# Optimization experiments

Measured on AMD Instinct MI355X. Metric: run time of the kernel, lower is better.

Reference implementation:

```python
import jax, jax.numpy as jnp
import numpy as np

N_NODES = 50000
N_PAIRS_MAP = 4096
N_EDGES = 500000
N_SCORE_PAIRS = 1000000
FEAT = 300   # feature_dim == in_channels
HID = 128    # hidden_channels
HEADS = 3
OUT = 10     # out_channels
NEG_SLOPE = 0.2


def setup_inputs() -> dict:
    key = jax.random.key(0)
    ks = jax.random.split(key, 24)
    s = 0.05
    d = {
        "feature_sub": jax.random.normal(ks[0], (N_PAIRS_MAP, FEAT), jnp.float32),
        "feature_com": jax.random.normal(ks[1], (N_PAIRS_MAP, FEAT), jnp.float32),
        "x": jax.random.normal(ks[2], (N_NODES, FEAT), jnp.float32),
        "com_idx": jax.random.randint(ks[3], (N_PAIRS_MAP,), 0, N_NODES, jnp.int32),
        "edge_index": jax.random.randint(ks[4], (2, N_EDGES), 0, N_NODES, jnp.int32),
        "pair_idx": jax.random.randint(ks[5], (N_SCORE_PAIRS, 2), 0, N_NODES, jnp.int32),
        # cross-attention params
        "Wq": jax.random.normal(ks[6], (FEAT, FEAT), jnp.float32) * s,
        "bq": jnp.zeros((FEAT,), jnp.float32),
        "Wk": jax.random.normal(ks[7], (FEAT, FEAT), jnp.float32) * s,
        "bk": jnp.zeros((FEAT,), jnp.float32),
        "Wv": jax.random.normal(ks[8], (FEAT, FEAT), jnp.float32) * s,
        "bv": jnp.zeros((FEAT,), jnp.float32),
        "Wf": jax.random.normal(ks[9], (FEAT, FEAT), jnp.float32) * s,
        "bf": jnp.zeros((FEAT,), jnp.float32),
        # GATConv layer 1 (heads=3, concat)
        "W1": jax.random.normal(ks[10], (FEAT, HEADS * HID), jnp.float32) * s,
        "a_src1": jax.random.normal(ks[11], (HEADS, HID), jnp.float32) * s,
        "a_dst1": jax.random.normal(ks[12], (HEADS, HID), jnp.float32) * s,
        "b1": jnp.zeros((HEADS * HID,), jnp.float32),
        # GATConv layer 2 (heads=1)
        "W2": jax.random.normal(ks[13], (HEADS * HID, OUT), jnp.float32) * s,
        "a_src2": jax.random.normal(ks[14], (1, OUT), jnp.float32) * s,
        "a_dst2": jax.random.normal(ks[15], (1, OUT), jnp.float32) * s,
        "b2": jnp.zeros((OUT,), jnp.float32),
    }
    return d


def gat_conv(h_in, src, dst, W, a_src, a_dst, b, n_nodes):
    """PyG-style GATConv: self-loops, per-dst softmax attention, sum-aggregate."""
    H, C = a_src.shape
    h = (h_in @ W).reshape(n_nodes, H, C)                     # [N,H,C]
    e_src = jnp.einsum("nhc,hc->nh", h, a_src)                # [N,H]
    e_dst = jnp.einsum("nhc,hc->nh", h, a_dst)                # [N,H]
    # add self-loops
    loops = jnp.arange(n_nodes, dtype=src.dtype)
    src = jnp.concatenate([src, loops])
    dst = jnp.concatenate([dst, loops])
    e = jax.nn.leaky_relu(e_src[src] + e_dst[dst], NEG_SLOPE)  # [E,H]
    m = jax.ops.segment_max(e, dst, num_segments=n_nodes)      # [N,H]
    m = jnp.where(jnp.isfinite(m), m, 0.0)
    ex = jnp.exp(e - m[dst])                                   # [E,H]
    denom = jax.ops.segment_sum(ex, dst, num_segments=n_nodes)  # [N,H]
    alpha = ex / (denom[dst] + 1e-16)                          # [E,H]
    msg = h[src] * alpha[..., None]                            # [E,H,C]
    out = jax.ops.segment_sum(msg, dst, num_segments=n_nodes)  # [N,H,C]
    return out.reshape(n_nodes, H * C) + b


def reference(feature_sub, feature_com, x, com_idx, edge_index, pair_idx,
              Wq, bq, Wk, bk, Wv, bv, Wf, bf,
              W1, a_src1, a_dst1, b1, W2, a_src2, a_dst2, b2):
    # --- compute_attention: cross-attention between sub and com features ---
    q = feature_sub @ Wq + bq                                  # [B,D]
    k = feature_com @ Wk + bk
    v = feature_com @ Wv + bv
    scores = jax.nn.softmax((q @ k.T) / jnp.sqrt(jnp.float32(FEAT)), axis=-1)
    fused = (feature_sub + scores @ v) @ Wf + bf               # [B,D]
    # --- change_node_feature: write fused features into graph node features ---
    x = x.at[com_idx].set(fused)
    # --- linkTrain: GAT1 -> ELU -> GAT2 ---
    src, dst = edge_index[0], edge_index[1]
    h = gat_conv(x, src, dst, W1, a_src1, a_dst1, b1, N_NODES)
    h = jax.nn.elu(h)
    emb = gat_conv(h, src, dst, W2, a_src2, a_dst2, b2, N_NODES)  # [N,OUT]
    # --- per-pair link scores (vectorized gather + batched dot) ---
    scores_out = jnp.sum(emb[pair_idx[:, 0]] * emb[pair_idx[:, 1]], axis=-1)
    return scores_out
```

## Files before the change

kernel.cpp:

```cpp
#include <hip/hip_runtime.h>
#include <math.h>

#define NN      50000
#define BP      4096
#define NE      500000
#define NP      1000000
#define FEAT    300
#define KP      320
#define HID     128
#define HEADS   3
#define OUTC    10
#define HC1     (HEADS*HID)
#define EMBS    12
#define TOTE    (NE+NN)
#define NEG_SLOPE 0.2f

static inline int cdiv(int a, int b) { return (a + b - 1) / b; }

using bfrag = __attribute__((ext_vector_type(8))) short;
using ffrag = __attribute__((ext_vector_type(4))) float;

__device__ inline float leaky(float x) { return x > 0.f ? x : NEG_SLOPE * x; }
__device__ inline unsigned short bf16_rne(float f) {
    unsigned u = __float_as_uint(f);
    unsigned r = u + 0x7FFFu + ((u >> 16) & 1u);
    return (unsigned short)(r >> 16);
}
__device__ inline float bf16f(unsigned short h) { return __uint_as_float(((unsigned)h) << 16); }

__device__ __forceinline__ void gload_lds16(const unsigned short* g, unsigned short* l) {
    __builtin_amdgcn_global_load_lds((const __attribute__((address_space(1))) void*)g,
                                     (__attribute__((address_space(3))) void*)l, 16, 0, 0);
}

__global__ void fill_f32(float* p, float v, long n) {
    long i = (long)blockIdx.x * blockDim.x + threadIdx.x;
    if (i < n) p[i] = v;
}

__global__ void conv_pad8(const float* __restrict__ in, unsigned short* __restrict__ H,
                          unsigned short* __restrict__ L, long M, int K, int Kp) {
    long idx = (long)blockIdx.x * blockDim.x + threadIdx.x;
    int cpk = Kp >> 3;
    long total = M * cpk;
    if (idx >= total) return;
    int chunk = (int)(idx % cpk);
    long row = idx / cpk;
    int k0 = chunk * 8;
    const float* ip = in + row * K;
    float v[8];
    if (k0 + 8 <= K) {
        float4 a = *(const float4*)(ip + k0);
        float4 b = *(const float4*)(ip + k0 + 4);
        v[0]=a.x; v[1]=a.y; v[2]=a.z; v[3]=a.w; v[4]=b.x; v[5]=b.y; v[6]=b.z; v[7]=b.w;
    } else {
#pragma unroll
        for (int j = 0; j < 8; j++) { int k = k0 + j; v[j] = (k < K) ? ip[k] : 0.f; }
    }
    unsigned short hs[8], ls[8];
#pragma unroll
    for (int j = 0; j < 8; j++) {
        unsigned short h = bf16_rne(v[j]);
        hs[j] = h; ls[j] = bf16_rne(v[j] - bf16f(h));
    }
    long o = row * Kp + k0;
    *(uint4*)&H[o] = *(const uint4*)hs;
    *(uint4*)&L[o] = *(const uint4*)ls;
}

__global__ void convT_pad(const float* __restrict__ in, unsigned short* __restrict__ H,
                          unsigned short* __restrict__ L, int K, int N, int Kp) {
    long idx = (long)blockIdx.x * blockDim.x + threadIdx.x;
    long total = (long)N * Kp;
    if (idx >= total) return;
    int k = (int)(idx % Kp);
    long n = idx / Kp;
    float f = (k < K) ? in[(long)k * N + n] : 0.f;
    unsigned short h = bf16_rne(f);
    H[idx] = h;
    L[idx] = bf16_rne(f - bf16f(h));
}

template <int MODE>
__global__ __launch_bounds__(256) void gemm_bf(
    const unsigned short* __restrict__ Ah, const unsigned short* __restrict__ Al, int lda,
    const unsigned short* __restrict__ Bh, const unsigned short* __restrict__ Bl, int ldb,
    const float* __restrict__ bias, const float* __restrict__ addsrc,
    float* __restrict__ C0, unsigned short* __restrict__ H0, unsigned short* __restrict__ L0,
    int M, int N, int K, float scale, int ldo)
{
    __shared__ __align__(16) unsigned short Ahs[4][64][8], Als[4][64][8];
    __shared__ __align__(16) unsigned short Bhs[4][64][8], Bls[4][64][8];
    int t = threadIdx.x, w = t >> 6, l = t & 63, lrow = l & 15, lq = l >> 4;
    int rowBase = blockIdx.y * 64, colBase = blockIdx.x * 64;
    int Kr = (K + 31) & ~31;

    int arow = min(rowBase + l, M - 1);
    int brow = min(colBase + l, N - 1);
    const unsigned short* ga_h = Ah + (long)arow * lda + w * 8;
    const unsigned short* ga_l = Al + (long)arow * lda + w * 8;
    const unsigned short* gb_h = Bh + (long)brow * ldb + w * 8;
    const unsigned short* gb_l = Bl + (long)brow * ldb + w * 8;

    ffrag acc[4] = {{0.f,0.f,0.f,0.f},{0.f,0.f,0.f,0.f},{0.f,0.f,0.f,0.f},{0.f,0.f,0.f,0.f}};

    for (int k0 = 0; k0 < Kr; k0 += 32) {
        *(uint4*)&Ahs[w][l][0] = *(const uint4*)(ga_h + k0);
        *(uint4*)&Als[w][l][0] = *(const uint4*)(ga_l + k0);
        *(uint4*)&Bhs[w][l][0] = *(const uint4*)(gb_h + k0);
        *(uint4*)&Bls[w][l][0] = *(const uint4*)(gb_l + k0);
        __syncthreads();
        bfrag ah  = *(const bfrag*)&Ahs[lq][w * 16 + lrow][0];
        bfrag alo = *(const bfrag*)&Als[lq][w * 16 + lrow][0];
#pragma unroll
        for (int ct = 0; ct < 4; ct++) {
            bfrag bh = *(const bfrag*)&Bhs[lq][ct * 16 + lrow][0];
            bfrag bl = *(const bfrag*)&Bls[lq][ct * 16 + lrow][0];
            acc[ct] = __builtin_amdgcn_mfma_f32_16x16x32_bf16(ah,  bh, acc[ct], 0, 0, 0);
            acc[ct] = __builtin_amdgcn_mfma_f32_16x16x32_bf16(ah,  bl, acc[ct], 0, 0, 0);
            acc[ct] = __builtin_amdgcn_mfma_f32_16x16x32_bf16(alo, bh, acc[ct], 0, 0, 0);
        }
        __syncthreads();
    }

#pragma unroll
    for (int ct = 0; ct < 4; ct++) {
        int gc = colBase + ct * 16 + lrow;
        if (gc >= N) continue;
#pragma unroll
        for (int r = 0; r < 4; r++) {
            int gr = rowBase + w * 16 + lq * 4 + r;
            if (gr >= M) continue;
            float v = acc[ct][r];
            if (MODE == 0) {
                float o = v * scale;
                if (bias) o += bias[gc];
                if (addsrc) o += addsrc[(long)gr * ldo + gc];
                C0[(long)gr * ldo + gc] = o;
            } else if (MODE == 1) {
                float o = v + bias[gc];
                unsigned short h = bf16_rne(o);
                H0[(long)gr * ldo + gc] = h;
                L0[(long)gr * ldo + gc] = bf16_rne(o - bf16f(h));
            } else {
                float o = v + bias[gc];
                unsigned short h = bf16_rne(o);
                H0[(long)gc * ldo + gr] = h;
                L0[(long)gc * ldo + gr] = bf16_rne(o - bf16f(h));
            }
        }
    }
}

template <bool SPLITK, int OUT>
__global__ __launch_bounds__(256) void gemm_gl128(
    const unsigned short* __restrict__ Ah, long dAl, int lda,
    const unsigned short* __restrict__ Bh, long dBl, int ldb,
    float* __restrict__ C0, unsigned short* __restrict__ Hb,
    int M, int N, int K, float scale, int KC)
{
    __shared__ __align__(16) unsigned short As[128][64];
    __shared__ __align__(16) unsigned short Bs[128][64];
    int t = threadIdx.x, w = t >> 6, l = t & 63, lrow = l & 15, lq = l >> 4;
    int wr = w >> 1, wc = w & 1;
    int rowBase = blockIdx.y * 128, colBase = blockIdx.x * 128;
    int Kr = (K + 31) & ~31;
    int kbeg = SPLITK ? blockIdx.z * KC : 0;
    int kend = SPLITK ? min(Kr, kbeg + KC) : Kr;

    bool isA = (w < 2);
    const unsigned short* Mb = isA ? Ah : Bh;
    long dHL = isA ? dAl : dBl;
    int ld   = isA ? lda : ldb;
    int mx   = (isA ? M : N) - 1;
    int rb0  = (isA ? rowBase : colBase) + (w & 1) * 64;
    int lr8  = l >> 3;
    int lg   = (l & 7) ^ lr8;
    long lane_off = (long)((lg & 3) * 8) + ((lg >> 2) ? dHL : 0);
    const unsigned short* gp[8];
#pragma unroll
    for (int i = 0; i < 8; i++) {
        int r = rb0 + i * 8 + lr8;
        gp[i] = Mb + (long)min(r, mx) * ld + lane_off;
    }
    unsigned short* ldst[8];
    {
        unsigned short (*T)[64] = isA ? As : Bs;
#pragma unroll
        for (int i = 0; i < 8; i++) ldst[i] = &T[(w & 1) * 64 + i * 8][0];
    }

    ffrag acc[4][4];
#pragma unroll
    for (int m = 0; m < 4; m++)
#pragma unroll
        for (int n = 0; n < 4; n++) acc[m][n] = ffrag{0.f, 0.f, 0.f, 0.f};

    int arow0 = wr * 64 + lrow, brow0 = wc * 64 + lrow;
    int xr = lrow & 7;
    int sh = ((lq    ) ^ xr) * 8;
    int sl = ((lq + 4) ^ xr) * 8;

    for (int k0 = kbeg; k0 < kend; k0 += 32) {
#pragma unroll
        for (int i = 0; i < 8; i++) gload_lds16(gp[i] + k0, ldst[i]);
        __syncthreads();

        bfrag bh[4], bl[4];
#pragma unroll
        for (int n = 0; n < 4; n++) {
            bh[n] = *(const bfrag*)&Bs[brow0 + n * 16][sh];
            bl[n] = *(const bfrag*)&Bs[brow0 + n * 16][sl];
        }
#pragma unroll
        for (int m = 0; m < 4; m++) {
            bfrag ah = *(const bfrag*)&As[arow0 + m * 16][sh];
            bfrag al = *(const bfrag*)&As[arow0 + m * 16][sl];
#pragma unroll
            for (int n = 0; n < 4; n++) {
                acc[m][n] = __builtin_amdgcn_mfma_f32_16x16x32_bf16(ah, bh[n], acc[m][n], 0, 0, 0);
                acc[m][n] = __builtin_amdgcn_mfma_f32_16x16x32_bf16(ah, bl[n], acc[m][n], 0, 0, 0);
                acc[m][n] = __builtin_amdgcn_mfma_f32_16x16x32_bf16(al, bh[n], acc[m][n], 0, 0, 0);
            }
        }
        __syncthreads();
    }

#pragma unroll
    for (int n = 0; n < 4; n++) {
        int gc = colBase + wc * 64 + n * 16 + lrow;
        if (gc >= N) continue;
#pragma unroll
        for (int m = 0; m < 4; m++) {
#pragma unroll
            for (int r = 0; r < 4; r++) {
                int gr = rowBase + wr * 64 + m * 16 + lq * 4 + r;
                if (gr >= M) continue;
                if (OUT == 0) {
                    float* Cz = SPLITK ? (C0 + (long)blockIdx.z * M * N) : C0;
                    Cz[(long)gr * N + gc] = acc[m][n][r] * scale;
                } else {
                    Hb[(long)gr * N + gc] = bf16_rne(acc[m][n][r]);
                }
            }
        }
    }
}

__global__ __launch_bounds__(256) void softmax_hl(const float* __restrict__ S,
                                                  unsigned short* __restrict__ SH,
                                                  unsigned short* __restrict__ SL) {
    int row = blockIdx.x, tid = threadIdx.x;
    const float* p = S + (long)row * BP + tid * 16;
    float ev[16];
    __shared__ float red[256];
    float m = -1e30f;
#pragma unroll
    for (int i = 0; i < 4; i++) {
        float4 a = *(const float4*)(p + i * 4);
        ev[4*i] = a.x; ev[4*i+1] = a.y; ev[4*i+2] = a.z; ev[4*i+3] = a.w;
        m = fmaxf(m, fmaxf(fmaxf(a.x, a.y), fmaxf(a.z, a.w)));
    }
    red[tid] = m; __syncthreads();
    for (int s = 128; s > 0; s >>= 1) { if (tid < s) red[tid] = fmaxf(red[tid], red[tid + s]); __syncthreads(); }
    m = red[0]; __syncthreads();
    float sum = 0.f;
#pragma unroll
    for (int i = 0; i < 16; i++) { float e = expf(ev[i] - m); ev[i] = e; sum += e; }
    red[tid] = sum; __syncthreads();
    for (int s = 128; s > 0; s >>= 1) { if (tid < s) red[tid] += red[tid + s]; __syncthreads(); }
    float inv = 1.0f / red[0];
    unsigned short hs[16], ls[16];
#pragma unroll
    for (int i = 0; i < 16; i++) {
        float e = ev[i] * inv;
        unsigned short h = bf16_rne(e);
        hs[i] = h; ls[i] = bf16_rne(e - bf16f(h));
    }
    long o = (long)row * BP + tid * 16;
    *(uint4*)&SH[o]     = *(const uint4*)&hs[0];
    *(uint4*)&SH[o + 8] = *(const uint4*)&hs[8];
    *(uint4*)&SL[o]     = *(const uint4*)&ls[0];
    *(uint4*)&SL[o + 8] = *(const uint4*)&ls[8];
}

__global__ void splitk_reduce8(const float* __restrict__ part, const float* __restrict__ resid,
                               unsigned short* __restrict__ H, unsigned short* __restrict__ L,
                               int Mr, int Nc, int Kp2, int sk) {
    long idx = (long)blockIdx.x * blockDim.x + threadIdx.x;
    int cpk = Kp2 >> 3;
    long total = (long)Mr * cpk;
    if (idx >= total) return;
    int chunk = (int)(idx % cpk);
    long row = idx / cpk;
    int c0 = chunk * 8;
    float v[8] = {0.f,0.f,0.f,0.f,0.f,0.f,0.f,0.f};
    if (c0 + 8 <= Nc) {
        long base = row * Nc + c0;
#pragma unroll
        for (int z = 0; z < 8; z++) {
            if (z >= sk) break;
            float4 a = *(const float4*)(part + (long)z * Mr * Nc + base);
            float4 b = *(const float4*)(part + (long)z * Mr * Nc + base + 4);
            v[0]+=a.x; v[1]+=a.y; v[2]+=a.z; v[3]+=a.w; v[4]+=b.x; v[5]+=b.y; v[6]+=b.z; v[7]+=b.w;
        }
        float4 a = *(const float4*)(resid + base);
        float4 b = *(const float4*)(resid + base + 4);
        v[0]+=a.x; v[1]+=a.y; v[2]+=a.z; v[3]+=a.w; v[4]+=b.x; v[5]+=b.y; v[6]+=b.z; v[7]+=b.w;
    } else if (c0 < Nc) {
#pragma unroll
        for (int j = 0; j < 8; j++) {
            int c = c0 + j;
            if (c < Nc) {
                long base = row * Nc + c;
                float s = resid[base];
                for (int z = 0; z < sk; z++) s += part[(long)z * Mr * Nc + base];
                v[j] = s;
            }
        }
    }
    unsigned short hs[8], ls[8];
#pragma unroll
    for (int j = 0; j < 8; j++) {
        unsigned short h = bf16_rne(v[j]);
        hs[j] = h; ls[j] = bf16_rne(v[j] - bf16f(h));
    }
    long o = row * Kp2 + c0;
    *(uint4*)&H[o] = *(const uint4*)hs;
    *(uint4*)&L[o] = *(const uint4*)ls;
}

__global__ void scatter_init(int* last, const int* __restrict__ com, int B) {
    int i = blockIdx.x * blockDim.x + threadIdx.x;
    if (i < B) last[com[i]] = -1;
}
__global__ void scatter_max(int* last, const int* __restrict__ com, int B) {
    int i = blockIdx.x * blockDim.x + threadIdx.x;
    if (i < B) atomicMax(&last[com[i]], i);
}
__global__ void scatter_write_hl(const int* __restrict__ last, const int* __restrict__ com,
                                 const float* __restrict__ fused,
                                 unsigned short* __restrict__ xH, unsigned short* __restrict__ xL, int B) {
    int i = blockIdx.x;
    int node = com[i];
    if (last[node] != i) return;
    for (int c = threadIdx.x; c < KP; c += blockDim.x) {
        float f = (c < FEAT) ? fused[(long)i * FEAT + c] : 0.f;
        unsigned short h = bf16_rne(f);
        xH[(long)node * KP + c] = h;
        xL[(long)node * KP + c] = bf16_rne(f - bf16f(h));
    }
}

__global__ __launch_bounds__(256) void node_attn_coef3(
    const unsigned short* __restrict__ h1, const float* __restrict__ a_src,
    const float* __restrict__ a_dst, float* __restrict__ es, float* __restrict__ ed, int N)
{
    int w = threadIdx.x >> 6, lane = threadIdx.x & 63;
    int n = blockIdx.x * 4 + w;
    if (n >= N) return;
    const unsigned short* hp = h1 + (long)n * HC1;
    float s0 = 0.f, s1 = 0.f, s2 = 0.f, d0 = 0.f, d1 = 0.f, d2 = 0.f;
#pragma unroll
    for (int j = 0; j < 2; j++) {
        int c = lane + 64 * j;
        float v = bf16f(hp[c]);
        s0 = fmaf(v, a_src[c], s0); d0 = fmaf(v, a_dst[c], d0);
        c += 128; v = bf16f(hp[c]);
        s1 = fmaf(v, a_src[c], s1); d1 = fmaf(v, a_dst[c], d1);
        c += 128; v = bf16f(hp[c]);
        s2 = fmaf(v, a_src[c], s2); d2 = fmaf(v, a_dst[c], d2);
    }
#pragma unroll
    for (int off = 32; off > 0; off >>= 1) {
        s0 += __shfl_down(s0, off); s1 += __shfl_down(s1, off); s2 += __shfl_down(s2, off);
        d0 += __shfl_down(d0, off); d1 += __shfl_down(d1, off); d2 += __shfl_down(d2, off);
    }
    if (lane == 0) {
        es[n * 3 + 0] = s0; es[n * 3 + 1] = s1; es[n * 3 + 2] = s2;
        ed[n * 3 + 0] = d0; ed[n * 3 + 1] = d1; ed[n * 3 + 2] = d2;
    }
}

__global__ void deg_init(int* deg, int n) {
    int i = blockIdx.x * blockDim.x + threadIdx.x;
    if (i < n) deg[i] = 1;
}
__global__ void deg_count(const int* __restrict__ dst, int* deg, int E) {
    int e = blockIdx.x * blockDim.x + threadIdx.x;
    if (e < E) atomicAdd(&deg[dst[e]], 1);
}
__global__ void scan_part(const int* __restrict__ deg, int* __restrict__ bsum, int n) {
    __shared__ int red[256];
    int tid = threadIdx.x;
    int i = blockIdx.x * 256 + tid;
    red[tid] = (i < n) ? deg[i] : 0;
    __syncthreads();
    for (int s = 128; s > 0; s >>= 1) { if (tid < s) red[tid] += red[tid + s]; __syncthreads(); }
    if (tid == 0) bsum[blockIdx.x] = red[0];
}
__global__ __launch_bounds__(256) void scan_bsum(int* __restrict__ bsum, int nb) {
    __shared__ int tmp[256];
    int tid = threadIdx.x;
    int v = (tid < nb) ? bsum[tid] : 0;
    tmp[tid] = v; __syncthreads();
    for (int off = 1; off < 256; off <<= 1) {
        int t2 = (tid >= off) ? tmp[tid - off] : 0;
        __syncthreads();
        tmp[tid] += t2;
        __syncthreads();
    }
    if (tid < nb) bsum[tid] = tmp[tid];
}
__global__ void scan_final(const int* __restrict__ deg, const int* __restrict__ bsum,
                           int* __restrict__ rowptr, int* __restrict__ curs, int n) {
    __shared__ int tmp[256];
    int tid = threadIdx.x;
    int b = blockIdx.x;
    int i = b * 256 + tid;
    int v = (i < n) ? deg[i] : 0;
    tmp[tid] = v; __syncthreads();
    for (int off = 1; off < 256; off <<= 1) {
        int t2 = (tid >= off) ? tmp[tid - off] : 0;
        __syncthreads();
        tmp[tid] += t2;
        __syncthreads();
    }
    int base = (b > 0) ? bsum[b - 1] : 0;
    if (i < n) {
        rowptr[i + 1] = base + tmp[tid];
        curs[i] = base + tmp[tid] - v;
    }
    if (b == 0 && tid == 0) rowptr[0] = 0;
}
__global__ void csr_fill(const int* __restrict__ src, const int* __restrict__ dst,
                         int* cursor, int* __restrict__ csr_src, int* __restrict__ csr_dst, int E) {
    int e = blockIdx.x * blockDim.x + threadIdx.x;
    if (e >= E) return;
    int d = dst[e];
    int slot = atomicAdd(&cursor[d], 1);
    csr_src[slot] = src[e];
    csr_dst[slot] = d;
}
__global__ void csr_fill_loops(int* cursor, int* __restrict__ csr_src, int* __restrict__ csr_dst, int n) {
    int i = blockIdx.x * blockDim.x + threadIdx.x;
    if (i >= n) return;
    int slot = atomicAdd(&cursor[i], 1);
    csr_src[slot] = i;
    csr_dst[slot] = i;
}

__global__ void edge_score3(const int* __restrict__ csr_src, const int* __restrict__ csr_dst,
                            const float* __restrict__ es, const float* __restrict__ ed,
                            float4* __restrict__ alpha, int E) {
    int s0 = blockIdx.x * blockDim.x + threadIdx.x;
    if (s0 >= E) return;
    int s = csr_src[s0], d = csr_dst[s0];
    float l0 = leaky(es[s * 3]     + ed[d * 3]);
    float l1 = leaky(es[s * 3 + 1] + ed[d * 3 + 1]);
    float l2 = leaky(es[s * 3 + 2] + ed[d * 3 + 2]);
    alpha[s0] = float4{l0, l1, l2, 0.f};
}
__global__ void seg_norm3(const int* __restrict__ rowptr, float4* __restrict__ alpha, int N) {
    int d = blockIdx.x * blockDim.x + threadIdx.x;
    if (d >= N) return;
    int b = rowptr[d], e = rowptr[d + 1];
    float m0 = -1e30f, m1 = -1e30f, m2 = -1e30f;
    for (int s0 = b; s0 < e; s0++) {
        float4 a = alpha[s0];
        m0 = fmaxf(m0, a.x); m1 = fmaxf(m1, a.y); m2 = fmaxf(m2, a.z);
    }
    float dn0 = 0.f, dn1 = 0.f, dn2 = 0.f;
    for (int s0 = b; s0 < e; s0++) {
        float4 a = alpha[s0];
        float x0 = expf(a.x - m0), x1 = expf(a.y - m1), x2 = expf(a.z - m2);
        dn0 += x0; dn1 += x1; dn2 += x2;
        alpha[s0] = float4{x0, x1, x2, 0.f};
    }
    float i0 = 1.f / (dn0 + 1e-16f), i1 = 1.f / (dn1 + 1e-16f), i2 = 1.f / (dn2 + 1e-16f);
    for (int s0 = b; s0 < e; s0++) {
        float4 a = alpha[s0];
        a.x *= i0; a.y *= i1; a.z *= i2;
        alpha[s0] = a;
    }
}

__global__ void csr_maxden_alpha1(const int* __restrict__ rowptr, const int* __restrict__ csr_src,
                                  const float* __restrict__ es, const float* __restrict__ ed,
                                  float* __restrict__ alpha, int N) {
    int d = blockIdx.x * blockDim.x + threadIdx.x;
    if (d >= N) return;
    float edv = ed[d];
    int b = rowptr[d], e = rowptr[d + 1];
    float mm = -1e30f;
    for (int s0 = b; s0 < e; s0++) {
        int s = csr_src[s0];
        mm = fmaxf(mm, leaky(es[s] + edv));
    }
    float dn = 0.f;
    for (int s0 = b; s0 < e; s0++) {
        int s = csr_src[s0];
        float ex = expf(leaky(es[s] + edv) - mm);
        dn += ex;
        alpha[s0] = ex;
    }
    float inv = 1.f / (dn + 1e-16f);
    for (int s0 = b; s0 < e; s0++) alpha[s0] *= inv;
}

__global__ __launch_bounds__(128) void csr_agg1_fused(
    const int* __restrict__ rowptr, const int* __restrict__ csr_src,
    const float4* __restrict__ alpha,
    const unsigned short* __restrict__ h1, const float* __restrict__ b1,
    const float* __restrict__ W2, float* __restrict__ h2,
    const float* __restrict__ as2, const float* __restrict__ ad2,
    float* __restrict__ es2, float* __restrict__ ed2, int N)
{
    int d = blockIdx.x;
    int t = threadIdx.x;
    __shared__ float row[HC1];
    __shared__ float part[128][OUTC + 1];

    int b = rowptr[d], e = rowptr[d + 1];
    float a0 = 0.f, a1 = 0.f, a2 = 0.f;

#define LOADG(g, I, A)                                                        \
    do {                                                                      \
        int base_ = b + (g) * 4;                                              \
        _Pragma("unroll")                                                     \
        for (int j = 0; j < 4; j++) {                                         \
            int s0_ = base_ + j;                                              \
            bool v_ = s0_ < e;                                                \
            int sc_ = v_ ? s0_ : (e - 1);                                     \
            I[j] = csr_src[sc_];                                              \
            float4 t4_ = alpha[sc_];                                          \
            if (!v_) { t4_.x = 0.f; t4_.y = 0.f; t4_.z = 0.f; }               \
            A[j] = t4_;                                                       \
        }                                                                     \
    } while (0)

    int ng = (e - b + 3) >> 2;
    int   iN[4]; float4 aN[4];
    LOADG(0, iN, aN);
    float rc[12]; float4 aC[4];
#pragma unroll
    for (int j = 0; j < 4; j++) {
        const unsigned short* hp = h1 + (long)iN[j] * HC1;
        rc[3 * j] = bf16f(hp[t]); rc[3 * j + 1] = bf16f(hp[t + 128]); rc[3 * j + 2] = bf16f(hp[t + 256]);
        aC[j] = aN[j];
    }
    LOADG(1, iN, aN);
    for (int g = 1; g < ng; g++) {
        float rn[12];
#pragma unroll
        for (int j = 0; j < 4; j++) {
            const unsigned short* hp = h1 + (long)iN[j] * HC1;
            rn[3 * j] = bf16f(hp[t]); rn[3 * j + 1] = bf16f(hp[t + 128]); rn[3 * j + 2] = bf16f(hp[t + 256]);
        }
        int iT[4]; float4 aT[4];
        LOADG(g + 1, iT, aT);
#pragma unroll
        for (int j = 0; j < 4; j++) {
            a0 = fmaf(rc[3 * j],     aC[j].x, a0);
            a1 = fmaf(rc[3 * j + 1], aC[j].y, a1);
            a2 = fmaf(rc[3 * j + 2], aC[j].z, a2);
        }
#pragma unroll
        for (int j = 0; j < 12; j++) rc[j] = rn[j];
#pragma unroll
        for (int j = 0; j < 4; j++) { aC[j] = aN[j]; iN[j] = iT[j]; aN[j] = aT[j]; }
    }
#pragma unroll
    for (int j = 0; j < 4; j++) {
        a0 = fmaf(rc[3 * j],     aC[j].x, a0);
        a1 = fmaf(rc[3 * j + 1], aC[j].y, a1);
        a2 = fmaf(rc[3 * j + 2], aC[j].z, a2);
    }
#undef LOADG

    float v;
    v = a0 + b1[t];       row[t]       = v > 0.f ? v : expf(v) - 1.f;
    v = a1 + b1[t + 128]; row[t + 128] = v > 0.f ? v : expf(v) - 1.f;
    v = a2 + b1[t + 256]; row[t + 256] = v > 0.f ? v : expf(v) - 1.f;
    __syncthreads();

    float pc[OUTC];
#pragma unroll
    for (int c = 0; c < OUTC; c++) pc[c] = 0.f;
    for (int k = t; k < HC1; k += 128) {
        float rv = row[k];
        const float* wp = W2 + (long)k * OUTC;
#pragma unroll
        for (int c = 0; c < OUTC; c++) pc[c] = fmaf(rv, wp[c], pc[c]);
    }
#pragma unroll
    for (int c = 0; c < OUTC; c++) part[t][c] = pc[c];
    __syncthreads();
    for (int off = 64; off > 0; off >>= 1) {
        if (t < off) {
#pragma unroll
            for (int c = 0; c < OUTC; c++) part[t][c] += part[t + off][c];
        }
        __syncthreads();
    }
    if (t < OUTC) h2[(long)d * OUTC + t] = part[0][t];
    if (t == 0) {
        float s = 0.f, dd = 0.f;
#pragma unroll
        for (int c = 0; c < OUTC; c++) {
            float hv = part[0][c];
            s  = fmaf(hv, as2[c], s);
            dd = fmaf(hv, ad2[c], dd);
        }
        es2[d] = s; ed2[d] = dd;
    }
}

__global__ void csr_agg2(const int* __restrict__ rowptr, const int* __restrict__ csr_src,
                         const float* __restrict__ alpha,
                         const float* __restrict__ h2, const float* __restrict__ b2,
                         float* __restrict__ emb, int N)
{
    int idx = blockIdx.x * blockDim.x + threadIdx.x;
    if (idx >= N * EMBS) return;
    int d = idx / EMBS, c = idx - d * EMBS;
    if (c >= OUTC) { emb[idx] = 0.f; return; }
    int b = rowptr[d], e = rowptr[d + 1];
    float acc = 0.f;
    for (int s0 = b; s0 < e; s0++) {
        int s = csr_src[s0];
        acc = fmaf(h2[(long)s * OUTC + c], alpha[s0], acc);
    }
    emb[idx] = acc + b2[c];
}

__global__ void pair_score(const int* __restrict__ pairs, const float* __restrict__ emb,
                           float* __restrict__ out, int P) {
    int p = blockIdx.x * blockDim.x + threadIdx.x;
    if (p >= P) return;
    int i0 = pairs[2 * p], i1 = pairs[2 * p + 1];
    const float4* a = (const float4*)(emb + (long)i0 * EMBS);
    const float4* b = (const float4*)(emb + (long)i1 * EMBS);
    float4 a0 = a[0], a1 = a[1], a2 = a[2];
    float4 b0 = b[0], b1 = b[1], b2 = b[2];
    float s = a0.x*b0.x + a0.y*b0.y + a0.z*b0.z + a0.w*b0.w
            + a1.x*b1.x + a1.y*b1.y + a1.z*b1.z + a1.w*b1.w
            + a2.x*b2.x + a2.y*b2.y;
    out[p] = s;
}

extern "C" void kernel_launch(void* const* d_in, const int* in_sizes, int n_in,
                              void* d_out, int out_size, void* d_ws, size_t ws_size,
                              hipStream_t stream) {
    const float* fsub = (const float*)d_in[0];
    const float* fcom = (const float*)d_in[1];
    float*       x    = (float*)d_in[2];
    const int*   com  = (const int*)d_in[3];
    const int*   ei   = (const int*)d_in[4];
    const int*   pidx = (const int*)d_in[5];
    const float* Wq = (const float*)d_in[6];  const float* bq = (const float*)d_in[7];
    const float* Wk = (const float*)d_in[8];  const float* bk = (const float*)d_in[9];
    const float* Wv = (const float*)d_in[10]; const float* bv = (const float*)d_in[11];
    const float* Wf = (const float*)d_in[12]; const float* bf = (const float*)d_in[13];
    const float* W1 = (const float*)d_in[14];
    const float* as1 = (const float*)d_in[15]; const float* ad1 = (const float*)d_in[16];
    const float* b1 = (const float*)d_in[17];
    const float* W2 = (const float*)d_in[18];
    const float* as2 = (const float*)d_in[19]; const float* ad2 = (const float*)d_in[20];
    const float* b2 = (const float*)d_in[21];
    float* out = (float*)d_out;

    const int* src = ei;
    const int* dst = ei + NE;

    typedef unsigned short u16;
    char* ws = (char*)d_ws;
    float* S     = (float*)(ws + 0);
    u16*   SH    = (u16*)(ws + 67108864);
    u16*   SL    = (u16*)(ws + 100663296);
    u16*   fsubH = (u16*)(ws + 134217728);
    u16*   fsubL = (u16*)(ws + 136839168);
    u16*   fcomH = (u16*)(ws + 139460608);
    u16*   fcomL = (u16*)(ws + 142082048);
    u16*   qH    = (u16*)(ws + 144703488);
    u16*   qL    = (u16*)(ws + 147324928);
    u16*   kH    = (u16*)(ws + 149946368);
    u16*   kL    = (u16*)(ws + 152567808);
    u16*   vTH   = (u16*)(ws + 155189248);
    u16*   vTL   = (u16*)(ws + 157646848);
    u16*   attnH = (u16*)(ws + 160104448);
    u16*   attnL = (u16*)(ws + 162725888);
    u16*   WqTH  = (u16*)(ws + 165347328);
    u16*   WqTL  = (u16*)(ws + 165539328);
    u16*   WkTH  = (u16*)(ws + 165731328);
    u16*   WkTL  = (u16*)(ws + 165923328);
    u16*   WvTH  = (u16*)(ws + 166115328);
    u16*   WvTL  = (u16*)(ws + 166307328);
    u16*   WfTH  = (u16*)(ws + 166499328);
    u16*   WfTL  = (u16*)(ws + 166691328);
    u16*   W1TH  = (u16*)(ws + 166883328);
    u16*   W1TL  = (u16*)(ws + 167129088);
    float* fus   = (float*)(ws + 167374848);
    float* es1   = (float*)(ws + 172290048);
    float* ed1   = (float*)(ws + 172890048);
    float* es2   = (float*)(ws + 174690048);
    float* ed2   = (float*)(ws + 174890048);
    float* h2    = (float*)(ws + 175490048);
    int*   last  = (int*)(ws + 179490048);
    int*   deg   = (int*)(ws + 179690048);
    int*   curs  = (int*)(ws + 179890048);
    int*   rowp  = (int*)(ws + 180090048);
    int*   csrc  = (int*)(ws + 180290064);
    int*   bsum  = (int*)(ws + 182490112);
    float* part   = (float*)(ws + 0);
    u16*   h1b    = (u16*)(ws + 0);
    u16*   xH     = (u16*)(ws + 76800000);
    u16*   xL     = (u16*)(ws + 108800000);
    float* alpha1 = (float*)(ws + 134217728);
    float* alpha2 = (float*)(ws + 144703488);
    int*   csrd   = (int*)(ws + 160104448);
    float* embp   = (float*)(ws + 147324928);

    const float inv_sqrt_d = 1.0f / sqrtf((float)FEAT);

    hipLaunchKernelGGL(convT_pad, dim3(cdiv(FEAT*KP,256)), dim3(256), 0, stream, Wq, WqTH, WqTL, FEAT, FEAT, KP);
    hipLaunchKernelGGL(convT_pad, dim3(cdiv(FEAT*KP,256)), dim3(256), 0, stream, Wk, WkTH, WkTL, FEAT, FEAT, KP);
    hipLaunchKernelGGL(convT_pad, dim3(cdiv(FEAT*KP,256)), dim3(256), 0, stream, Wv, WvTH, WvTL, FEAT, FEAT, KP);
    hipLaunchKernelGGL(convT_pad, dim3(cdiv(FEAT*KP,256)), dim3(256), 0, stream, Wf, WfTH, WfTL, FEAT, FEAT, KP);
    hipLaunchKernelGGL(convT_pad, dim3(cdiv(HC1*KP,256)),  dim3(256), 0, stream, W1, W1TH, W1TL, FEAT, HC1, KP);
    hipLaunchKernelGGL(conv_pad8, dim3(cdiv(BP*(KP/8),256)), dim3(256), 0, stream, fsub, fsubH, fsubL, BP, FEAT, KP);
    hipLaunchKernelGGL(conv_pad8, dim3(cdiv(BP*(KP/8),256)), dim3(256), 0, stream, fcom, fcomH, fcomL, BP, FEAT, KP);
    hipLaunchKernelGGL(fill_f32, dim3(cdiv(10485760/4,256)), dim3(256), 0, stream, (float*)qH, 0.f, (long)(10485760/4));

    hipLaunchKernelGGL((gemm_bf<1>), dim3(cdiv(FEAT,64), cdiv(BP,64)), dim3(256), 0, stream,
                       fsubH, fsubL, KP, WqTH, WqTL, KP, bq, nullptr, nullptr, qH, qL,
                       BP, FEAT, FEAT, 1.0f, KP);
    hipLaunchKernelGGL((gemm_bf<1>), dim3(cdiv(FEAT,64), cdiv(BP,64)), dim3(256), 0, stream,
                       fcomH, fcomL, KP, WkTH, WkTL, KP, bk, nullptr, nullptr, kH, kL,
                       BP, FEAT, FEAT, 1.0f, KP);
    hipLaunchKernelGGL((gemm_bf<2>), dim3(cdiv(FEAT,64), cdiv(BP,64)), dim3(256), 0, stream,
                       fcomH, fcomL, KP, WvTH, WvTL, KP, bv, nullptr, nullptr, vTH, vTL,
                       BP, FEAT, FEAT, 1.0f, BP);
    hipLaunchKernelGGL((gemm_gl128<false, 0>), dim3(cdiv(BP,128), cdiv(BP,128)), dim3(256), 0, stream,
                       qH, (long)(qL - qH), KP, kH, (long)(kL - kH), KP,
                       S, nullptr, BP, BP, FEAT, inv_sqrt_d, 0);
    hipLaunchKernelGGL(softmax_hl, dim3(BP), dim3(256), 0, stream, S, SH, SL);
    hipLaunchKernelGGL((gemm_gl128<true, 0>), dim3(cdiv(FEAT,128), cdiv(BP,128), 4), dim3(256), 0, stream,
                       SH, (long)(SL - SH), BP, vTH, (long)(vTL - vTH), BP,
                       part, nullptr, BP, FEAT, BP, 1.0f, 1024);
    hipLaunchKernelGGL(splitk_reduce8, dim3(cdiv(BP*(KP/8),256)), dim3(256), 0, stream,
                       part, fsub, attnH, attnL, BP, FEAT, KP, 4);
    hipLaunchKernelGGL((gemm_bf<0>), dim3(cdiv(FEAT,64), cdiv(BP,64)), dim3(256), 0, stream,
                       attnH, attnL, KP, WfTH, WfTL, KP, bf, nullptr, fus, nullptr, nullptr,
                       BP, FEAT, FEAT, 1.0f, FEAT);

    hipLaunchKernelGGL(conv_pad8, dim3(cdiv((long)NN*(KP/8),256)), dim3(256), 0, stream, x, xH, xL, NN, FEAT, KP);
    hipLaunchKernelGGL(scatter_init, dim3(cdiv(BP,256)), dim3(256), 0, stream, last, com, BP);
    hipLaunchKernelGGL(scatter_max,  dim3(cdiv(BP,256)), dim3(256), 0, stream, last, com, BP);
    hipLaunchKernelGGL(scatter_write_hl, dim3(BP), dim3(128), 0, stream, last, com, fus, xH, xL, BP);

    hipLaunchKernelGGL(deg_init,  dim3(cdiv(NN,256)), dim3(256), 0, stream, deg, NN);
    hipLaunchKernelGGL(deg_count, dim3(cdiv(NE,256)), dim3(256), 0, stream, dst, deg, NE);
    {
        int nb = cdiv(NN, 256);
        hipLaunchKernelGGL(scan_part,  dim3(nb), dim3(256), 0, stream, deg, bsum, NN);
        hipLaunchKernelGGL(scan_bsum,  dim3(1),  dim3(256), 0, stream, bsum, nb);
        hipLaunchKernelGGL(scan_final, dim3(nb), dim3(256), 0, stream, deg, bsum, rowp, curs, NN);
    }
    hipLaunchKernelGGL(csr_fill, dim3(cdiv(NE,256)), dim3(256), 0, stream, src, dst, curs, csrc, csrd, NE);
    hipLaunchKernelGGL(csr_fill_loops, dim3(cdiv(NN,256)), dim3(256), 0, stream, curs, csrc, csrd, NN);

    hipLaunchKernelGGL((gemm_gl128<false, 1>), dim3(cdiv(HC1,128), cdiv(NN,128)), dim3(256), 0, stream,
                       xH, (long)(xL - xH), KP, W1TH, (long)(W1TL - W1TH), KP,
                       nullptr, h1b, NN, HC1, FEAT, 1.0f, 0);
    hipLaunchKernelGGL(node_attn_coef3, dim3(cdiv(NN,4)), dim3(256), 0, stream,
                       h1b, as1, ad1, es1, ed1, NN);
    hipLaunchKernelGGL(edge_score3, dim3(cdiv(TOTE,256)), dim3(256), 0, stream,
                       csrc, csrd, es1, ed1, (float4*)alpha1, TOTE);
    hipLaunchKernelGGL(seg_norm3, dim3(cdiv(NN,256)), dim3(256), 0, stream,
                       rowp, (float4*)alpha1, NN);
    hipLaunchKernelGGL(csr_agg1_fused, dim3(NN), dim3(128), 0, stream,
                       rowp, csrc, (const float4*)alpha1, h1b, b1, W2, h2, as2, ad2, es2, ed2, NN);

    hipLaunchKernelGGL(csr_maxden_alpha1, dim3(cdiv(NN,256)), dim3(256), 0, stream,
                       rowp, csrc, es2, ed2, alpha2, NN);
    hipLaunchKernelGGL(csr_agg2, dim3(cdiv(NN*EMBS,256)), dim3(256), 0, stream,
                       rowp, csrc, alpha2, h2, b2, embp, NN);

    hipLaunchKernelGGL(pair_score, dim3(cdiv(NP,256)), dim3(256), 0, stream, pidx, embp, out, NP);
}
```

Before: 722.4 us.

## Use paired bf16 loads in GAT attention coef and aggregation kernels

The node attention coefficient kernel now reads two bf16 values per lane with one 32-bit load instead of six scalar 16-bit loads. The layer-1 aggregation kernel moves from 128 to 192 threads, each thread loading a packed bf16 pair per neighbor. It drops the 4-deep software-pipelined gather loop for a simple per-edge loop, and the shared-memory reduction is reworked to fit 192 threads. This cuts the number of load instructions and widens each access, but gives up the explicit prefetching of neighbor indices and rows and adds a barrier.

```diff
diff --git a/kernel.cpp b/kernel.cpp
--- a/kernel.cpp
+++ b/kernel.cpp
@@ -27,6 +27,8 @@
     return (unsigned short)(r >> 16);
 }
 __device__ inline float bf16f(unsigned short h) { return __uint_as_float(((unsigned)h) << 16); }
+__device__ inline float bf16lo(unsigned u) { return __uint_as_float(u << 16); }
+__device__ inline float bf16hi(unsigned u) { return __uint_as_float(u & 0xffff0000u); }
 
 __device__ __forceinline__ void gload_lds16(const unsigned short* g, unsigned short* l) {
     __builtin_amdgcn_global_load_lds((const __attribute__((address_space(1))) void*)g,
@@ -360,16 +362,21 @@
     int n = blockIdx.x * 4 + w;
     if (n >= N) return;
     const unsigned short* hp = h1 + (long)n * HC1;
-    float s0 = 0.f, s1 = 0.f, s2 = 0.f, d0 = 0.f, d1 = 0.f, d2 = 0.f;
-#pragma unroll
-    for (int j = 0; j < 2; j++) {
-        int c = lane + 64 * j;
-        float v = bf16f(hp[c]);
-        s0 = fmaf(v, a_src[c], s0); d0 = fmaf(v, a_dst[c], d0);
-        c += 128; v = bf16f(hp[c]);
-        s1 = fmaf(v, a_src[c], s1); d1 = fmaf(v, a_dst[c], d1);
-        c += 128; v = bf16f(hp[c]);
-        s2 = fmaf(v, a_src[c], s2); d2 = fmaf(v, a_dst[c], d2);
+    int c = 2 * lane;
+    unsigned u0 = *(const unsigned*)&hp[c];
+    unsigned u1 = *(const unsigned*)&hp[128 + c];
+    unsigned u2 = *(const unsigned*)&hp[256 + c];
+    float s0, s1, s2, d0, d1, d2;
+    {
+        float vl = bf16lo(u0), vh = bf16hi(u0);
+        s0 = fmaf(vl, a_src[c], vh * a_src[c + 1]);
+        d0 = fmaf(vl, a_dst[c], vh * a_dst[c + 1]);
+        vl = bf16lo(u1); vh = bf16hi(u1);
+        s1 = fmaf(vl, a_src[128 + c], vh * a_src[128 + c + 1]);
+        d1 = fmaf(vl, a_dst[128 + c], vh * a_dst[128 + c + 1]);
+        vl = bf16lo(u2); vh = bf16hi(u2);
+        s2 = fmaf(vl, a_src[256 + c], vh * a_src[256 + c + 1]);
+        d2 = fmaf(vl, a_dst[256 + c], vh * a_dst[256 + c + 1]);
     }
 #pragma unroll
     for (int off = 32; off > 0; off >>= 1) {
@@ -508,7 +515,7 @@
     for (int s0 = b; s0 < e; s0++) alpha[s0] *= inv;
 }
 
-__global__ __launch_bounds__(128) void csr_agg1_fused(
+__global__ __launch_bounds__(192) void csr_agg1_fused(
     const int* __restrict__ rowptr, const int* __restrict__ csr_src,
     const float4* __restrict__ alpha,
     const unsigned short* __restrict__ h1, const float* __restrict__ b1,
@@ -519,75 +526,32 @@
     int d = blockIdx.x;
     int t = threadIdx.x;
     __shared__ float row[HC1];
-    __shared__ float part[128][OUTC + 1];
+    __shared__ float part[192][OUTC + 1];
 
     int b = rowptr[d], e = rowptr[d + 1];
-    float a0 = 0.f, a1 = 0.f, a2 = 0.f;
-
-#define LOADG(g, I, A)                                                        \
-    do {                                                                      \
-        int base_ = b + (g) * 4;                                              \
-        _Pragma("unroll")                                                     \
-        for (int j = 0; j < 4; j++) {                                         \
-            int s0_ = base_ + j;                                              \
-            bool v_ = s0_ < e;                                                \
-            int sc_ = v_ ? s0_ : (e - 1);                                     \
-            I[j] = csr_src[sc_];                                              \
-            float4 t4_ = alpha[sc_];                                          \
-            if (!v_) { t4_.x = 0.f; t4_.y = 0.f; t4_.z = 0.f; }               \
-            A[j] = t4_;                                                       \
-        }                                                                     \
-    } while (0)
-
-    int ng = (e - b + 3) >> 2;
-    int   iN[4]; float4 aN[4];
-    LOADG(0, iN, aN);
-    float rc[12]; float4 aC[4];
-#pragma unroll
-    for (int j = 0; j < 4; j++) {
-        const unsigned short* hp = h1 + (long)iN[j] * HC1;
-        rc[3 * j] = bf16f(hp[t]); rc[3 * j + 1] = bf16f(hp[t + 128]); rc[3 * j + 2] = bf16f(hp[t + 256]);
-        aC[j] = aN[j];
-    }
-    LOADG(1, iN, aN);
-    for (int g = 1; g < ng; g++) {
-        float rn[12];
-#pragma unroll
-        for (int j = 0; j < 4; j++) {
-            const unsigned short* hp = h1 + (long)iN[j] * HC1;
-            rn[3 * j] = bf16f(hp[t]); rn[3 * j + 1] = bf16f(hp[t + 128]); rn[3 * j + 2] = bf16f(hp[t + 256]);
-        }
-        int iT[4]; float4 aT[4];
-        LOADG(g + 1, iT, aT);
-#pragma unroll
-        for (int j = 0; j < 4; j++) {
-            a0 = fmaf(rc[3 * j],     aC[j].x, a0);
-            a1 = fmaf(rc[3 * j + 1], aC[j].y, a1);
-            a2 = fmaf(rc[3 * j + 2], aC[j].z, a2);
-        }
-#pragma unroll
-        for (int j = 0; j < 12; j++) rc[j] = rn[j];
-#pragma unroll
-        for (int j = 0; j < 4; j++) { aC[j] = aN[j]; iN[j] = iT[j]; aN[j] = aT[j]; }
-    }
-#pragma unroll
-    for (int j = 0; j < 4; j++) {
-        a0 = fmaf(rc[3 * j],     aC[j].x, a0);
-        a1 = fmaf(rc[3 * j + 1], aC[j].y, a1);
-        a2 = fmaf(rc[3 * j + 2], aC[j].z, a2);
-    }
-#undef LOADG
-
-    float v;
-    v = a0 + b1[t];       row[t]       = v > 0.f ? v : expf(v) - 1.f;
-    v = a1 + b1[t + 128]; row[t + 128] = v > 0.f ? v : expf(v) - 1.f;
-    v = a2 + b1[t + 256]; row[t + 256] = v > 0.f ? v : expf(v) - 1.f;
+    int c0 = 2 * t;
+    int hsel = t >> 6;
+    float a0 = 0.f, a1 = 0.f;
+
+    for (int s0 = b; s0 < e; s0++) {
+        int s = csr_src[s0];
+        float4 al4 = alpha[s0];
+        unsigned u = *(const unsigned*)&h1[(long)s * HC1 + c0];
+        float av = (hsel == 0) ? al4.x : ((hsel == 1) ? al4.y : al4.z);
+        a0 = fmaf(bf16lo(u), av, a0);
+        a1 = fmaf(bf16hi(u), av, a1);
+    }
+
+    float v0 = a0 + b1[c0];
+    float v1 = a1 + b1[c0 + 1];
+    row[c0]     = v0 > 0.f ? v0 : expf(v0) - 1.f;
+    row[c0 + 1] = v1 > 0.f ? v1 : expf(v1) - 1.f;
     __syncthreads();
 
     float pc[OUTC];
 #pragma unroll
     for (int c = 0; c < OUTC; c++) pc[c] = 0.f;
-    for (int k = t; k < HC1; k += 128) {
+    for (int k = t; k < HC1; k += 192) {
         float rv = row[k];
         const float* wp = W2 + (long)k * OUTC;
 #pragma unroll
@@ -596,14 +560,19 @@
 #pragma unroll
     for (int c = 0; c < OUTC; c++) part[t][c] = pc[c];
     __syncthreads();
-    for (int off = 64; off > 0; off >>= 1) {
+    for (int off = 96; off > 5; off >>= 1) {
         if (t < off) {
 #pragma unroll
             for (int c = 0; c < OUTC; c++) part[t][c] += part[t + off][c];
         }
         __syncthreads();
     }
-    if (t < OUTC) h2[(long)d * OUTC + t] = part[0][t];
+    if (t < OUTC) {
+        float hv = part[0][t] + part[1][t] + part[2][t] + part[3][t] + part[4][t] + part[5][t];
+        h2[(long)d * OUTC + t] = hv;
+        part[0][t] = hv;
+    }
+    __syncthreads();
     if (t == 0) {
         float s = 0.f, dd = 0.f;
 #pragma unroll
@@ -779,7 +748,7 @@
                        csrc, csrd, es1, ed1, (float4*)alpha1, TOTE);
     hipLaunchKernelGGL(seg_norm3, dim3(cdiv(NN,256)), dim3(256), 0, stream,
                        rowp, (float4*)alpha1, NN);
-    hipLaunchKernelGGL(csr_agg1_fused, dim3(NN), dim3(128), 0, stream,
+    hipLaunchKernelGGL(csr_agg1_fused, dim3(NN), dim3(192), 0, stream,
                        rowp, csrc, (const float4*)alpha1, h1b, b1, W2, h2, as2, ad2, es2, ed2, NN);
 
     hipLaunchKernelGGL(csr_maxden_alpha1, dim3(cdiv(NN,256)), dim3(256), 0, stream,
```

New measurement: 765.4 us. +6.0%, slower.
